# Kernel optimization log

Hardware: AMD Instinct MI355X
Metric: run time of the kernel (lower is better)

The kernel has to match this reference:

```python
import jax, jax.numpy as jnp
import numpy as np
from jax import lax

V, E, H = 128, 32, 128  # vocab, embed_dim, hidden_size
B, S = 4, 512


def setup_inputs() -> dict:
    key = jax.random.key(0)
    ks = jax.random.split(key, 14)
    sc = 0.05
    return {
        "x": jax.random.randint(ks[0], (B, S), 0, V),
        "emb": jax.random.normal(ks[1], (V, E), jnp.float32) * sc,
        "W_ih": jax.random.normal(ks[2], (4 * H, E), jnp.float32) * sc,
        "W_hh": jax.random.normal(ks[3], (4 * H, H), jnp.float32) * sc,
        "b_ih": jax.random.normal(ks[4], (4 * H,), jnp.float32) * sc,
        "b_hh": jax.random.normal(ks[5], (4 * H,), jnp.float32) * sc,
        "Wq": jax.random.normal(ks[6], (H, H), jnp.float32) * sc,
        "bq": jax.random.normal(ks[7], (H,), jnp.float32) * sc,
        "Wk": jax.random.normal(ks[8], (H, H), jnp.float32) * sc,
        "bk": jax.random.normal(ks[9], (H,), jnp.float32) * sc,
        "v": jax.random.normal(ks[10], (H,), jnp.float32) * sc,
        "Wf": jax.random.normal(ks[11], (V, 2 * H), jnp.float32) * sc,
        "bf": jax.random.normal(ks[12], (V,), jnp.float32) * sc,
    }


def _lstm(e, W_ih, W_hh, b_ih, b_hh):
    # e: (B, S, E) -> outputs (B, S, H); PyTorch gate order i, f, g, o
    b, s, _ = e.shape
    h0 = jnp.zeros((b, H), e.dtype)
    c0 = jnp.zeros((b, H), e.dtype)
    bias = b_ih + b_hh

    def step(carry, xt):
        h, c = carry
        g = xt @ W_ih.T + h @ W_hh.T + bias  # (B, 4H)
        i, f, gg, o = jnp.split(g, 4, axis=-1)
        c = jax.nn.sigmoid(f) * c + jax.nn.sigmoid(i) * jnp.tanh(gg)
        h = jax.nn.sigmoid(o) * jnp.tanh(c)
        return (h, c), h

    (hT, cT), hs = lax.scan(step, (h0, c0), jnp.swapaxes(e, 0, 1))
    return jnp.swapaxes(hs, 0, 1), hT, cT


def reference(x, emb, W_ih, W_hh, b_ih, b_hh, Wq, bq, Wk, bk, v, Wf, bf):
    e = emb[x]  # (B, S, E)
    out, hT, cT = _lstm(e, W_ih, W_hh, b_ih, b_hh)  # (B, S, H)
    s = out.shape[1]
    q = out @ Wq.T + bq  # (B, S, H)
    k = out @ Wk.T + bk  # (B, S, H)
    # Bahdanau additive scores: v^T tanh(q_t + k_i) -> (B, S, S)
    t = jnp.tanh(q[:, :, None, :] + k[:, None, :, :])  # (B, S, S, H)
    scores = jnp.einsum('bsth,h->bst', t, v)
    mask = jnp.tril(jnp.ones((s, s), bool))
    scores = jnp.where(mask[None], scores, -jnp.inf)
    w = jax.nn.softmax(scores, axis=-1)
    ctx = jnp.einsum('bst,bth->bsh', w, out)
    logits = jnp.concatenate([out, ctx], axis=-1) @ Wf.T + bf  # (B, S, V)
    return logits, hT, cT
```

## Files before the change

### kernel.cpp

```cpp
#include <hip/hip_runtime.h>

#define Vn 128
#define En 32
#define Hn 128
#define Bn 4
#define Sn 512
#define G4H 512

typedef _Float16 half8 __attribute__((ext_vector_type(8)));
typedef float    floatx4 __attribute__((ext_vector_type(4)));

__device__ __forceinline__ float fsigmoid(float x) {
    return 1.0f / (1.0f + __expf(-x));
}

__device__ __forceinline__ float ftanh(float x) {
    float e = __expf(2.0f * x);
    return 1.0f - 2.0f / (e + 1.0f);
}

__global__ __launch_bounds__(512) void k_gtab(
        const float* __restrict__ emb, const float* __restrict__ Wih,
        const float* __restrict__ bih, const float* __restrict__ bhh,
        float* __restrict__ Gtab) {
    int v = blockIdx.x;
    int g = threadIdx.x;
    __shared__ float e[En];
    if (g < En) e[g] = emb[v * En + g];
    __syncthreads();
    const float4* wr = (const float4*)(Wih + g * En);
    float acc = bih[g] + bhh[g];
#pragma unroll
    for (int i = 0; i < En / 4; i++) {
        float4 w4 = wr[i];
        acc += w4.x * e[4*i] + w4.y * e[4*i+1] + w4.z * e[4*i+2] + w4.w * e[4*i+3];
    }
    Gtab[v * G4H + (g & 127) * 4 + (g >> 7)] = acc;
}

__global__ __attribute__((amdgpu_flat_work_group_size(512, 512),
                          amdgpu_waves_per_eu(2, 2)))
void k_lstm(
        const float* __restrict__ Whh, const float* __restrict__ Gtab,
        const int* __restrict__ x,
        float* __restrict__ out, float* __restrict__ hT, float* __restrict__ cT) {
    int tid = threadIdx.x;
    int wv  = tid >> 6;
    int l   = tid & 63;
    int cn  = l & 15;
    int kg  = l >> 4;
    int cb  = l & 3;
    int jr  = l >> 2;
    int bb  = l & 3;
    int aj  = 16 * wv + jr;

    bool r1 = (l >> 2) & 1;
    bool r2 = (l >> 2) & 2;

    __shared__ int xb[4][520];
    __shared__ alignas(16) _Float16 hbuf[2][4][144];

    for (int i = tid; i < Bn * Sn; i += 512) xb[i >> 9][i & 511] = x[i] * 2048;
    if (tid < 4) xb[tid][512] = 0;
    for (int i = tid; i < 2 * 4 * 144; i += 512) ((_Float16*)hbuf)[i] = (_Float16)0.0f;

    half8 af[4][4];
#pragma unroll
    for (int g = 0; g < 4; g++) {
#pragma unroll
        for (int kc = 0; kc < 4; kc++) {
            int row = g * Hn + 16 * wv + cn;
            int kb  = kc * 32 + kg * 8;
            const float4* p = (const float4*)(Whh + row * Hn + kb);
            float4 lo = p[0], hi = p[1];
            half8 a = { (_Float16)lo.x, (_Float16)lo.y, (_Float16)lo.z, (_Float16)lo.w,
                        (_Float16)hi.x, (_Float16)hi.y, (_Float16)hi.z, (_Float16)hi.w };
            af[g][kc] = a;
        }
    }

    float c_ = 0.f, h_ = 0.f;
    const char* gbase = (const char*)Gtab + aj * 16;
    float* outp = out + bb * Sn * Hn + aj;
    __syncthreads();

    float4 gx4 = *(const float4*)(gbase + xb[bb][0]);

#pragma unroll 2
    for (int s = 0; s < Sn; s++) {
        half8 bf[4];
#pragma unroll
        for (int kc = 0; kc < 4; kc++)
            bf[kc] = *(const half8*)&hbuf[s & 1][cb][kc * 32 + kg * 8];

        floatx4 d[4];
#pragma unroll
        for (int g = 0; g < 4; g++) {
            floatx4 acc = { 0.f, 0.f, 0.f, 0.f };
#pragma unroll
            for (int kc = 0; kc < 4; kc++)
                acc = __builtin_amdgcn_mfma_f32_16x16x32_f16(af[g][kc], bf[kc], acc, 0, 0, 0);
            d[g] = acc;
        }

        float4 ngx = *(const float4*)(gbase + xb[bb][s + 1]);

        float ex[4];
#pragma unroll
        for (int g = 0; g < 4; g++) {
            float lo = r1 ? d[g][1] : d[g][0];
            float hi = r1 ? d[g][3] : d[g][2];
            ex[g] = r2 ? hi : lo;
        }

        float gi = gx4.x + ex[0];
        float gf = gx4.y + ex[1];
        float gg = gx4.z + ex[2];
        float go = gx4.w + ex[3];
        c_ = fsigmoid(gf) * c_ + fsigmoid(gi) * ftanh(gg);
        h_ = fsigmoid(go) * ftanh(c_);

        *outp = h_;  outp += Hn;
        hbuf[(s & 1) ^ 1][bb][aj] = (_Float16)h_;

        gx4 = ngx;
        asm volatile("s_waitcnt lgkmcnt(0)\n\ts_barrier" ::: "memory");
    }
    hT[bb * Hn + aj] = h_;
    cT[bb * Hn + aj] = c_;
}

__global__ __launch_bounds__(128) void k_k(
        const float* __restrict__ out, const float* __restrict__ Wk,
        const float* __restrict__ bk, float* __restrict__ ko) {
    int bs  = blockIdx.x;
    int tid = threadIdx.x;
    __shared__ float o[Hn];
    o[tid] = out[bs * Hn + tid];
    __syncthreads();
    const float4* wr = (const float4*)(Wk + tid * Hn);
    float acc = bk[tid];
#pragma unroll
    for (int i = 0; i < Hn / 4; i++) {
        float4 w4 = wr[i];
        acc += w4.x * o[4*i] + w4.y * o[4*i+1] + w4.z * o[4*i+2] + w4.w * o[4*i+3];
    }
    ko[bs * Hn + tid] = acc;
}

__global__ __launch_bounds__(512) void k_attn(
        const float* __restrict__ ko, const float* __restrict__ vvec,
        const float* __restrict__ out,
        const float* __restrict__ Wq, const float* __restrict__ bq,
        const float* __restrict__ Wf, const float* __restrict__ bf,
        float* __restrict__ logits) {
    int b   = blockIdx.x >> 9;
    int t   = blockIdx.x & (Sn - 1);
    int tid = threadIdx.x;
    int wv  = tid >> 6;
    __shared__ float qs[Hn];
    __shared__ float vs[Hn];
    __shared__ float oc[2 * Hn];
    __shared__ float sc[Sn];
    __shared__ float wmax[8];
    __shared__ float wsum[8];
    __shared__ float part[16][Hn];

    if (tid < Hn) {
        oc[tid] = out[(b * Sn + t) * Hn + tid];
        vs[tid] = vvec[tid];
    }
    __syncthreads();

    {
        int h = tid & 127, kq = tid >> 7;
        const float4* wr = (const float4*)(Wq + h * Hn + kq * 32);
        const float* ob = oc + kq * 32;
        float a = 0.0f;
#pragma unroll
        for (int i = 0; i < 8; i++) {
            float4 w4 = wr[i];
            a += w4.x * ob[4*i] + w4.y * ob[4*i+1] + w4.z * ob[4*i+2] + w4.w * ob[4*i+3];
        }
        part[kq][h] = a;
    }
    __syncthreads();
    if (tid < Hn)
        qs[tid] = bq[tid] + part[0][tid] + part[1][tid] + part[2][tid] + part[3][tid];
    __syncthreads();

    float a = -1e30f;
    if (tid <= t) {
        const float4* kr = (const float4*)(ko + (b * Sn + tid) * Hn);
        float s = 0.0f;
#pragma unroll
        for (int u = 0; u < Hn / 4; u++) {
            float4 k4 = kr[u];
            s += vs[4*u]   * ftanh(qs[4*u]   + k4.x);
            s += vs[4*u+1] * ftanh(qs[4*u+1] + k4.y);
            s += vs[4*u+2] * ftanh(qs[4*u+2] + k4.z);
            s += vs[4*u+3] * ftanh(qs[4*u+3] + k4.w);
        }
        sc[tid] = s;
        a = s;
    }
#pragma unroll
    for (int off = 32; off > 0; off >>= 1) a = fmaxf(a, __shfl_xor(a, off));
    if ((tid & 63) == 0) wmax[wv] = a;
    __syncthreads();
    float m = wmax[0];
#pragma unroll
    for (int r = 1; r < 8; r++) m = fmaxf(m, wmax[r]);

    float ev = 0.0f;
    if (tid <= t) {
        ev = __expf(sc[tid] - m);
        sc[tid] = ev;
    }
    float ssum = ev;
#pragma unroll
    for (int off = 32; off > 0; off >>= 1) ssum += __shfl_xor(ssum, off);
    if ((tid & 63) == 0) wsum[wv] = ssum;
    __syncthreads();
    float tot = wsum[0];
#pragma unroll
    for (int r = 1; r < 8; r++) tot += wsum[r];
    float inv = 1.0f / tot;

    int hq = tid & 31;
    int is = tid >> 5;
    float4 acc = {0.0f, 0.0f, 0.0f, 0.0f};
    const float4* ob4 = (const float4*)(out + b * Sn * Hn);
    for (int i = is; i <= t; i += 16) {
        float s = sc[i];
        float4 o4 = ob4[i * (Hn / 4) + hq];
        acc.x += s * o4.x; acc.y += s * o4.y;
        acc.z += s * o4.z; acc.w += s * o4.w;
    }
    ((float4*)part[is])[hq] = acc;
    __syncthreads();
    if (tid < Hn) {
        float sum2 = 0.0f;
#pragma unroll
        for (int r = 0; r < 16; r++) sum2 += part[r][tid];
        oc[Hn + tid] = sum2 * inv;
    }
    __syncthreads();

    {
        int v = tid & 127, kq = tid >> 7;
        const float4* wr = (const float4*)(Wf + v * 2 * Hn + kq * 64);
        const float* ob = oc + kq * 64;
        float a2 = 0.0f;
#pragma unroll
        for (int i = 0; i < 16; i++) {
            float4 w4 = wr[i];
            a2 += w4.x * ob[4*i] + w4.y * ob[4*i+1] + w4.z * ob[4*i+2] + w4.w * ob[4*i+3];
        }
        part[kq][v] = a2;
    }
    __syncthreads();
    if (tid < Hn)
        logits[(b * Sn + t) * Vn + tid] =
            bf[tid] + part[0][tid] + part[1][tid] + part[2][tid] + part[3][tid];
}

extern "C" void kernel_launch(void* const* d_in, const int* in_sizes, int n_in,
                              void* d_out, int out_size, void* d_ws, size_t ws_size,
                              hipStream_t stream) {
    const int*   x   = (const int*)d_in[0];
    const float* emb = (const float*)d_in[1];
    const float* Wih = (const float*)d_in[2];
    const float* Whh = (const float*)d_in[3];
    const float* bih = (const float*)d_in[4];
    const float* bhh = (const float*)d_in[5];
    const float* Wq  = (const float*)d_in[6];
    const float* bq  = (const float*)d_in[7];
    const float* Wk  = (const float*)d_in[8];
    const float* bk  = (const float*)d_in[9];
    const float* v   = (const float*)d_in[10];
    const float* Wf  = (const float*)d_in[11];
    const float* bf  = (const float*)d_in[12];

    float* logits = (float*)d_out;
    float* hT     = logits + Bn * Sn * Vn;
    float* cT     = hT + Bn * Hn;

    float* ws   = (float*)d_ws;
    float* Gtab = ws;
    float* outb = ws + 65536;
    float* ko   = ws + 65536 + 262144;

    k_gtab<<<Vn, 512, 0, stream>>>(emb, Wih, bih, bhh, Gtab);
    k_lstm<<<1, 512, 0, stream>>>(Whh, Gtab, x, outb, hT, cT);
    k_k<<<Bn * Sn, 128, 0, stream>>>(outb, Wk, bk, ko);
    k_attn<<<Bn * Sn, 512, 0, stream>>>(ko, v, outb, Wq, bq, Wf, bf, logits);
}
```

Baseline: 518.0 us.

## Split LSTM MFMA chain into two accumulators and transpose key layout for coalescing

In the sequential LSTM step, the four dependent MFMA accumulations per gate are split into two independent chains that are summed at the end. This shortens the dependency latency on the critical recurrent path. The key projection output is also stored in a transposed float4-interleaved layout (b, h/4, s, 4), so that neighbouring threads in the attention score loop read neighbouring addresses and the loads coalesce. The cost is an extra vector add per gate and scattered stores in the key kernel.

```diff
diff --git a/kernel.cpp b/kernel.cpp
--- a/kernel.cpp
+++ b/kernel.cpp
@@ -96,11 +96,13 @@
         floatx4 d[4];
 #pragma unroll
         for (int g = 0; g < 4; g++) {
-            floatx4 acc = { 0.f, 0.f, 0.f, 0.f };
-#pragma unroll
-            for (int kc = 0; kc < 4; kc++)
-                acc = __builtin_amdgcn_mfma_f32_16x16x32_f16(af[g][kc], bf[kc], acc, 0, 0, 0);
-            d[g] = acc;
+            floatx4 a0 = { 0.f, 0.f, 0.f, 0.f };
+            floatx4 a1 = { 0.f, 0.f, 0.f, 0.f };
+            a0 = __builtin_amdgcn_mfma_f32_16x16x32_f16(af[g][0], bf[0], a0, 0, 0, 0);
+            a1 = __builtin_amdgcn_mfma_f32_16x16x32_f16(af[g][2], bf[2], a1, 0, 0, 0);
+            a0 = __builtin_amdgcn_mfma_f32_16x16x32_f16(af[g][1], bf[1], a0, 0, 0, 0);
+            a1 = __builtin_amdgcn_mfma_f32_16x16x32_f16(af[g][3], bf[3], a1, 0, 0, 0);
+            d[g] = a0 + a1;
         }
 
         float4 ngx = *(const float4*)(gbase + xb[bb][s + 1]);
@@ -132,8 +134,10 @@
 
 __global__ __launch_bounds__(128) void k_k(
         const float* __restrict__ out, const float* __restrict__ Wk,
-        const float* __restrict__ bk, float* __restrict__ ko) {
+        const float* __restrict__ bk, float* __restrict__ koT) {
     int bs  = blockIdx.x;
+    int b   = bs >> 9;
+    int s   = bs & (Sn - 1);
     int tid = threadIdx.x;
     __shared__ float o[Hn];
     o[tid] = out[bs * Hn + tid];
@@ -145,11 +149,11 @@
         float4 w4 = wr[i];
         acc += w4.x * o[4*i] + w4.y * o[4*i+1] + w4.z * o[4*i+2] + w4.w * o[4*i+3];
     }
-    ko[bs * Hn + tid] = acc;
+    koT[b * 65536 + (tid >> 2) * 2048 + s * 4 + (tid & 3)] = acc;
 }
 
 __global__ __launch_bounds__(512) void k_attn(
-        const float* __restrict__ ko, const float* __restrict__ vvec,
+        const float* __restrict__ koT, const float* __restrict__ vvec,
         const float* __restrict__ out,
         const float* __restrict__ Wq, const float* __restrict__ bq,
         const float* __restrict__ Wf, const float* __restrict__ bf,
@@ -191,11 +195,11 @@
 
     float a = -1e30f;
     if (tid <= t) {
-        const float4* kr = (const float4*)(ko + (b * Sn + tid) * Hn);
+        const float4* kT = (const float4*)koT + b * 16384 + tid;
         float s = 0.0f;
 #pragma unroll
         for (int u = 0; u < Hn / 4; u++) {
-            float4 k4 = kr[u];
+            float4 k4 = kT[u * 512];
             s += vs[4*u]   * ftanh(qs[4*u]   + k4.x);
             s += vs[4*u+1] * ftanh(qs[4*u+1] + k4.y);
             s += vs[4*u+2] * ftanh(qs[4*u+2] + k4.z);
@@ -289,10 +293,10 @@
     float* ws   = (float*)d_ws;
     float* Gtab = ws;
     float* outb = ws + 65536;
-    float* ko   = ws + 65536 + 262144;
+    float* koT  = ws + 65536 + 262144;
 
     k_gtab<<<Vn, 512, 0, stream>>>(emb, Wih, bih, bhh, Gtab);
     k_lstm<<<1, 512, 0, stream>>>(Whh, Gtab, x, outb, hT, cT);
-    k_k<<<Bn * Sn, 128, 0, stream>>>(outb, Wk, bk, ko);
-    k_attn<<<Bn * Sn, 512, 0, stream>>>(ko, v, outb, Wq, bq, Wf, bf, logits);
-}
+    k_k<<<Bn * Sn, 128, 0, stream>>>(outb, Wk, bk, koT);
+    k_attn<<<Bn * Sn, 512, 0, stream>>>(koT, v, outb, Wq, bq, Wf, bf, logits);
+}
```

After: 564.8 us. 9.0% more time.
